# Kernel tuning notes

Hardware: AMD Instinct MI355X
Metric: run time of the kernel (lower is better)

Reference implementation:

```python
import jax, jax.numpy as jnp
import numpy as np

D = 512
H = 8
DH = D // H  # 64


def setup_inputs() -> dict:
    key = jax.random.key(0)
    ks = jax.random.split(key, 7)
    batch, la, lb = 8, 256, 256
    A = jax.random.normal(ks[0], (batch, la, D), dtype=jnp.float32)
    B = jax.random.normal(ks[1], (batch, lb, D), dtype=jnp.float32)
    s = 1.0 / np.sqrt(D)
    W1 = jax.random.uniform(ks[2], (D, D), minval=-s, maxval=s, dtype=jnp.float32)
    b1 = jax.random.uniform(ks[3], (D,), minval=-s, maxval=s, dtype=jnp.float32)
    W2 = jax.random.uniform(ks[4], (D, D), minval=-s, maxval=s, dtype=jnp.float32)
    b2 = jax.random.uniform(ks[5], (D,), minval=-s, maxval=s, dtype=jnp.float32)
    q = jax.random.normal(ks[6], (DH,), dtype=jnp.float32) * 0.1
    return {"A": A, "B": B, "W1": W1, "b1": b1, "W2": W2, "b2": b2, "q": q}


def reference(A, B, W1, b1, W2, b2, q):
    bs, la, _ = A.shape
    lb = B.shape[1]
    # Linear + ReLU, then raw row-major reshape to (batch, heads, len, dh)
    # (matches torch .view semantics: NOT a head-transpose split)
    A_ = jax.nn.relu(A @ W1.T + b1).reshape(bs, H, la, DH)
    B_ = jax.nn.relu(B @ W2.T + b2).reshape(bs, H, lb, DH)
    # bilinear score: tanh of elementwise pairwise product, dotted with q
    # att_maps: [bs, H, la, lb]
    att_maps = jnp.einsum(
        "bhijc,c->bhij",
        jnp.tanh(A_[:, :, :, None, :] * B_[:, :, None, :, :]),
        q,
    )
    temp_b2a = jax.nn.softmax(jnp.mean(att_maps, axis=3), axis=2)  # [bs,H,la]
    temp_a2b = jax.nn.softmax(jnp.mean(att_maps, axis=2), axis=2)  # [bs,H,lb]
    A_heads = A.reshape(bs, H, la, DH)
    B_heads = B.reshape(bs, H, lb, DH)
    A_p = jnp.sum(A_heads * temp_b2a[..., None], axis=2).reshape(bs, -1)  # [bs, d]
    B_p = jnp.sum(B_heads * temp_a2b[..., None], axis=2).reshape(bs, -1)  # [bs, d]
    return (
        jnp.concatenate((A_p, B_p), axis=1),
        jnp.mean(temp_b2a, axis=1),
        jnp.mean(temp_a2b, axis=1),
    )
```

## Files before the change

kernel.cpp:

```cpp
#include <hip/hip_runtime.h>
#include <hip/hip_bf16.h>

#define LOG2E 1.4426950408889634f
#define CHEB_R 4.0f
#define CHEB_M 40
#define CHEB_P 80
#define PI_F 3.14159265358979f

typedef __attribute__((ext_vector_type(8))) short short8b;
typedef __attribute__((ext_vector_type(4))) short short4b;
typedef __attribute__((ext_vector_type(4))) float f32x4;

__device__ __forceinline__ float fast_exp2(float x) {
#if __has_builtin(__builtin_amdgcn_exp2f)
  return __builtin_amdgcn_exp2f(x);
#else
  return exp2f(x);
#endif
}
__device__ __forceinline__ float fast_rcp(float x) {
#if __has_builtin(__builtin_amdgcn_rcpf)
  return __builtin_amdgcn_rcpf(x);
#else
  return 1.0f / x;
#endif
}
__device__ __forceinline__ short f2bf(float f) {
  __hip_bfloat16 h = __float2bfloat16(f);
  return *reinterpret_cast<short*>(&h);
}

__global__ __launch_bounds__(256) void gemm_kernel(
    const float* __restrict__ Xa, const float* __restrict__ Wa,
    const float* __restrict__ ba, float* __restrict__ Oa,
    const float* __restrict__ Xb, const float* __restrict__ Wb,
    const float* __restrict__ bb, float* __restrict__ Ob) {
  const int isB = blockIdx.z;
  const float* X = isB ? Xb : Xa;
  const float* W = isB ? Wb : Wa;
  const float* bias = isB ? bb : ba;
  float* O = isB ? Ob : Oa;

  __shared__ __align__(16) short As[64 * 40];
  __shared__ __align__(16) short Ws[64 * 40];

  int t = threadIdx.x;
  int m0 = blockIdx.x * 64, n0 = blockIdx.y * 64;
  int l = t & 63, w = t >> 6;
  int wm = (w >> 1) * 32, wn = (w & 1) * 32;
  int lr = l & 15, ko = (l >> 4) * 8;

  f32x4 acc[2][2];
#pragma unroll
  for (int m = 0; m < 2; ++m)
#pragma unroll
    for (int n = 0; n < 2; ++n) acc[m][n] = f32x4{0.f, 0.f, 0.f, 0.f};

  for (int k0 = 0; k0 < 512; k0 += 32) {
#pragma unroll
    for (int s = 0; s < 2; ++s) {
      int slot = t + s * 256;
      int row = slot >> 3, qd = (slot & 7) << 2;
      float4 v = *reinterpret_cast<const float4*>(&X[(m0 + row) * 512 + k0 + qd]);
      short4b sv = {f2bf(v.x), f2bf(v.y), f2bf(v.z), f2bf(v.w)};
      *reinterpret_cast<short4b*>(&As[row * 40 + qd]) = sv;
      float4 u = *reinterpret_cast<const float4*>(&W[(n0 + row) * 512 + k0 + qd]);
      short4b su = {f2bf(u.x), f2bf(u.y), f2bf(u.z), f2bf(u.w)};
      *reinterpret_cast<short4b*>(&Ws[row * 40 + qd]) = su;
    }
    __syncthreads();

    short8b afr[2], bfr[2];
#pragma unroll
    for (int m = 0; m < 2; ++m)
      afr[m] = *reinterpret_cast<const short8b*>(&As[(wm + m * 16 + lr) * 40 + ko]);
#pragma unroll
    for (int n = 0; n < 2; ++n)
      bfr[n] = *reinterpret_cast<const short8b*>(&Ws[(wn + n * 16 + lr) * 40 + ko]);
#pragma unroll
    for (int m = 0; m < 2; ++m)
#pragma unroll
      for (int n = 0; n < 2; ++n)
        acc[m][n] = __builtin_amdgcn_mfma_f32_16x16x32_bf16(afr[m], bfr[n], acc[m][n], 0, 0, 0);
    __syncthreads();
  }

#pragma unroll
  for (int n = 0; n < 2; ++n) {
    int col = n0 + wn + n * 16 + lr;
    float bv = bias[col];
#pragma unroll
    for (int m = 0; m < 2; ++m) {
      int rbase = m0 + wm + m * 16 + (l >> 4) * 4;
#pragma unroll
      for (int r = 0; r < 4; ++r) {
        float v = acc[m][n][r] + bv;
        O[(rbase + r) * 512 + col] = v > 0.f ? v : 0.f;
      }
    }
  }
}

__global__ __launch_bounds__(256) void moments_kernel(
    const float* __restrict__ Ar, const float* __restrict__ Br,
    float* __restrict__ Fpart, float* __restrict__ Gpart,
    float* __restrict__ cmn) {
  __shared__ __align__(16) float smem[13056];

  int t = threadIdx.x;

  if (blockIdx.x == 64) {
    if (blockIdx.y != 0 || blockIdx.z != 0) return;
    float* S = smem;
    float* T = smem + 6400;
    float* H = smem + 9600;
    for (int e = t; e < 6400; e += 256) {
      int p = e >> 6 ? e / 80 : e / 80;
      p = e / 80;
      int qq = e - p * 80;
      float xp = CHEB_R * 0.5f * (1.f + cosf((2.f * p + 1.f) * (PI_F / 160.f)));
      float xq = CHEB_R * 0.5f * (1.f + cosf((2.f * qq + 1.f) * (PI_F / 160.f)));
      S[e] = tanhf(xp * xq);
    }
    for (int e = t; e < CHEB_M * 80; e += 256) {
      int n = e / 80, qq = e - n * 80;
      T[e] = cosf((float)n * (2.f * qq + 1.f) * (PI_F / 160.f));
    }
    __syncthreads();
    for (int e = t; e < CHEB_M * 80; e += 256) {
      int n = e / 80, p = e - n * 80;
      float s = 0.f;
      for (int qq = 0; qq < 80; ++qq) s = fmaf(T[n * 80 + qq], S[p * 80 + qq], s);
      H[n * 80 + p] = s;
    }
    __syncthreads();
    for (int e = t; e < CHEB_M * CHEB_M; e += 256) {
      int m = e / CHEB_M, n = e - m * CHEB_M;
      float s = 0.f;
      for (int p = 0; p < 80; ++p) s = fmaf(T[m * 80 + p], H[n * 80 + p], s);
      float wm = (m == 0) ? 1.f : 2.f;
      float wn = (n == 0) ? 1.f : 2.f;
      cmn[e] = s * (wm * wn / 6400.f);
    }
    return;
  }

  float* red = smem;
  int bh = blockIdx.x, half = blockIdx.y, quad = blockIdx.z;
  const float* X = half ? Br : Ar;
  float* Out = half ? Gpart : Fpart;
  int c = t & 63, colsel = t >> 6;
  int colhi = quad * 2 + (colsel & 1);
  int rowh = colsel >> 1;
  int rbase = (bh >> 3) * 256 + (bh & 7) * 32 + rowh * 16;
  const float* p = X + rbase * 512 + colhi * 64 + c;

  float acc[CHEB_M];
#pragma unroll
  for (int m = 0; m < CHEB_M; ++m) acc[m] = 0.f;

#pragma unroll 1
  for (int rr = 0; rr < 16; ++rr) {
    float a = p[rr * 512];
    float u = fminf(a * (2.f / CHEB_R) - 1.f, 1.f);
    float tp = 1.f, tc = u;
    acc[0] += 1.f;
    acc[1] += u;
#pragma unroll
    for (int m = 2; m < CHEB_M; ++m) {
      float tn = fmaf(2.f * u, tc, -tp);
      acc[m] += tn;
      tp = tc; tc = tn;
    }
  }
#pragma unroll
  for (int m = 0; m < CHEB_M; ++m) red[(colsel * CHEB_M + m) * 64 + c] = acc[m];
  __syncthreads();
  for (int e = t; e < CHEB_M * 64; e += 256) {
    int m = e >> 6, cc = e & 63;
    float s = red[(0 * CHEB_M + m) * 64 + cc] + red[(1 * CHEB_M + m) * 64 + cc] +
              red[(2 * CHEB_M + m) * 64 + cc] + red[(3 * CHEB_M + m) * 64 + cc];
    Out[(((bh * 4 + quad) * CHEB_M) + m) * 64 + cc] = s;
  }
}

__global__ __launch_bounds__(512) void finalize_kernel(
    const float* __restrict__ Ar, const float* __restrict__ Br,
    const float* __restrict__ Fpart, const float* __restrict__ Gpart,
    const float* __restrict__ cmn, const float* __restrict__ q,
    float* __restrict__ rowmean, float* __restrict__ colmean) {
  __shared__ float cs[CHEB_M * CHEB_M];
  __shared__ float Fs[CHEB_M * 64];
  __shared__ float Gs[CHEB_M * 64];
  __shared__ float gq[CHEB_M * 64];
  __shared__ float dq[CHEB_M * 64];

  int bh = blockIdx.x, qd = blockIdx.y;
  int t = threadIdx.x;

  for (int e = t; e < CHEB_M * CHEB_M; e += 512) cs[e] = cmn[e];
  for (int e = t; e < CHEB_M * 64; e += 512) {
    float f = 0.f, g = 0.f;
#pragma unroll
    for (int p = 0; p < 4; ++p) {
      f += Fpart[((bh * 4 + p) * CHEB_M) * 64 + e];
      g += Gpart[((bh * 4 + p) * CHEB_M) * 64 + e];
    }
    Fs[e] = f; Gs[e] = g;
  }
  __syncthreads();

  for (int e = t; e < CHEB_M * 64; e += 512) {
    int m = e >> 6, c = e & 63;
    float qc = q[c] * (1.f / 256.f);
    float sg = 0.f, sd = 0.f;
    for (int n = 0; n < CHEB_M; ++n) {
      sg = fmaf(cs[m * CHEB_M + n], Gs[n * 64 + c], sg);
      sd = fmaf(cs[n * CHEB_M + m], Fs[n * 64 + c], sd);
    }
    gq[e] = sg * qc;
    dq[e] = sd * qc;
  }
  __syncthreads();

  int rbase = (bh >> 3) * 256 + (bh & 7) * 32;
  {
    int i = qd * 64 + (t >> 3);
    int ce = t & 7;
    const float* base = Ar + (rbase + (i >> 3)) * 512 + (i & 7) * 64;
    float s = 0.f;
#pragma unroll 1
    for (int cc = 0; cc < 8; ++cc) {
      int c = ce * 8 + cc;
      float a = base[c];
      float u = fminf(a * (2.f / CHEB_R) - 1.f, 1.f);
      float tp = 1.f, tc = u;
      s += gq[0 * 64 + c];
      s = fmaf(gq[1 * 64 + c], u, s);
#pragma unroll
      for (int m = 2; m < CHEB_M; ++m) {
        float tn = fmaf(2.f * u, tc, -tp);
        s = fmaf(gq[m * 64 + c], tn, s);
        tp = tc; tc = tn;
      }
    }
    s += __shfl_xor(s, 1);
    s += __shfl_xor(s, 2);
    s += __shfl_xor(s, 4);
    if ((t & 7) == 0) rowmean[bh * 256 + i] = s;
  }
  {
    int j = qd * 64 + (t >> 3);
    int ce = t & 7;
    const float* base = Br + (rbase + (j >> 3)) * 512 + (j & 7) * 64;
    float s = 0.f;
#pragma unroll 1
    for (int cc = 0; cc < 8; ++cc) {
      int c = ce * 8 + cc;
      float b = base[c];
      float u = fminf(b * (2.f / CHEB_R) - 1.f, 1.f);
      float tp = 1.f, tc = u;
      s += dq[0 * 64 + c];
      s = fmaf(dq[1 * 64 + c], u, s);
#pragma unroll
      for (int m = 2; m < CHEB_M; ++m) {
        float tn = fmaf(2.f * u, tc, -tp);
        s = fmaf(dq[m * 64 + c], tn, s);
        tp = tc; tc = tn;
      }
    }
    s += __shfl_xor(s, 1);
    s += __shfl_xor(s, 2);
    s += __shfl_xor(s, 4);
    if ((t & 7) == 0) colmean[bh * 256 + j] = s;
  }
}

__global__ __launch_bounds__(512) void softmax_pool_kernel(
    const float* __restrict__ rowmean, const float* __restrict__ colmean,
    const float* __restrict__ A0, const float* __restrict__ B0,
    float* __restrict__ b2a, float* __restrict__ a2b,
    float* __restrict__ poolA, float* __restrict__ poolB) {
  int bh = blockIdx.x, chunk = blockIdx.y;
  int b = bh >> 3, h = bh & 7;
  int t = threadIdx.x;
  int tt = t & 255;
  int lane = t & 63, w = (t >> 6) & 3;
  __shared__ float redA[4], redB[4], redC[4], redD[4];
  __shared__ float tA[256], tB[256];
  __shared__ float pp[8][64];

  float r = rowmean[bh * 256 + tt];
  float cs = colmean[bh * 256 + tt];

  float mr = r, mc = cs;
#pragma unroll
  for (int off = 32; off >= 1; off >>= 1) {
    mr = fmaxf(mr, __shfl_xor(mr, off));
    mc = fmaxf(mc, __shfl_xor(mc, off));
  }
  if (lane == 0) { redA[w] = mr; redB[w] = mc; }
  __syncthreads();
  mr = fmaxf(fmaxf(redA[0], redA[1]), fmaxf(redA[2], redA[3]));
  mc = fmaxf(fmaxf(redB[0], redB[1]), fmaxf(redB[2], redB[3]));

  float er = fast_exp2((r - mr) * LOG2E);
  float ec = fast_exp2((cs - mc) * LOG2E);
  float sr = er, sc = ec;
#pragma unroll
  for (int off = 32; off >= 1; off >>= 1) {
    sr += __shfl_xor(sr, off);
    sc += __shfl_xor(sc, off);
  }
  if (lane == 0) { redC[w] = sr; redD[w] = sc; }
  __syncthreads();
  sr = redC[0] + redC[1] + redC[2] + redC[3];
  sc = redD[0] + redD[1] + redD[2] + redD[3];

  float vb2a = er * fast_rcp(sr);
  float va2b = ec * fast_rcp(sc);
  tA[tt] = vb2a; tB[tt] = va2b;
  if (chunk == 0) {
    b2a[bh * 256 + tt] = vb2a;
    a2b[bh * 256 + tt] = va2b;
  }
  __syncthreads();

  int c = t & 63, isub = t >> 6;
  const float* Ab = A0 + b * 131072 + h * 16384;
  const float* Bb = B0 + b * 131072 + h * 16384;
  float pa = 0.f, pb = 0.f;
#pragma unroll
  for (int ii = 0; ii < 8; ++ii) {
    int i = chunk * 64 + isub * 8 + ii;
    pa = fmaf(Ab[i * 64 + c], tA[i], pa);
    pb = fmaf(Bb[i * 64 + c], tB[i], pb);
  }
  pp[isub][c] = pa;
  __syncthreads();
  if (t < 64) {
    float s = 0.f;
#pragma unroll
    for (int k = 0; k < 8; ++k) s += pp[k][t];
    poolA[(bh * 4 + chunk) * 64 + t] = s;
  }
  __syncthreads();
  pp[isub][c] = pb;
  __syncthreads();
  if (t < 64) {
    float s = 0.f;
#pragma unroll
    for (int k = 0; k < 8; ++k) s += pp[k][t];
    poolB[(bh * 4 + chunk) * 64 + t] = s;
  }
}

__global__ __launch_bounds__(256) void final_kernel(
    const float* __restrict__ poolA, const float* __restrict__ poolB,
    const float* __restrict__ b2a, const float* __restrict__ a2b,
    float* __restrict__ out) {
  int b = blockIdx.x, t = threadIdx.x;
  float s1 = 0.f, s2 = 0.f;
#pragma unroll
  for (int h = 0; h < 8; ++h) {
    s1 += b2a[(b * 8 + h) * 256 + t];
    s2 += a2b[(b * 8 + h) * 256 + t];
  }
  out[8192 + b * 256 + t] = s1 * 0.125f;
  out[10240 + b * 256 + t] = s2 * 0.125f;

#pragma unroll
  for (int hh = 0; hh < 2; ++hh) {
    int idx = hh * 256 + t;
    int h = idx >> 6, c = idx & 63;
    int base = ((b * 8 + h) * 4) * 64 + c;
    float sA = poolA[base] + poolA[base + 64] + poolA[base + 128] + poolA[base + 192];
    float sB = poolB[base] + poolB[base + 64] + poolB[base + 128] + poolB[base + 192];
    out[b * 1024 + h * 64 + c] = sA;
    out[b * 1024 + 512 + h * 64 + c] = sB;
  }
}

extern "C" void kernel_launch(void* const* d_in, const int* in_sizes, int n_in,
                              void* d_out, int out_size, void* d_ws, size_t ws_size,
                              hipStream_t stream) {
  const float* A  = (const float*)d_in[0];
  const float* B  = (const float*)d_in[1];
  const float* W1 = (const float*)d_in[2];
  const float* b1 = (const float*)d_in[3];
  const float* W2 = (const float*)d_in[4];
  const float* b2 = (const float*)d_in[5];
  const float* q  = (const float*)d_in[6];
  float* out = (float*)d_out;
  float* ws = (float*)d_ws;

  float* Ar      = ws;
  float* Br      = ws + 1048576;
  float* Fpart   = ws + 2097152;
  float* Gpart   = ws + 2752512;
  float* cmn     = ws + 3407872;
  float* rowmean = ws + 3409472;
  float* colmean = ws + 3425856;
  float* b2a     = ws + 3442240;
  float* a2b     = ws + 3458624;
  float* poolA   = ws + 3475008;
  float* poolB   = ws + 3491392;

  gemm_kernel<<<dim3(32, 8, 2), 256, 0, stream>>>(A, W1, b1, Ar, B, W2, b2, Br);
  moments_kernel<<<dim3(65, 2, 4), 256, 0, stream>>>(Ar, Br, Fpart, Gpart, cmn);
  finalize_kernel<<<dim3(64, 4), 512, 0, stream>>>(Ar, Br, Fpart, Gpart, cmn, q,
                                                   rowmean, colmean);
  softmax_pool_kernel<<<dim3(64, 4), 512, 0, stream>>>(
      rowmean, colmean, A, B, b2a, a2b, poolA, poolB);
  final_kernel<<<8, 256, 0, stream>>>(poolA, poolB, b2a, a2b, out);
}
```

Before: 70.99 us.

## Move Chebyshev coefficient setup into GEMM launch and interleave recurrences for ILP

The one-block computation of the tanh Chebyshev coefficient matrix moves from the moments kernel into an extra z-slice of the GEMM launch. It now runs alongside the GEMM and no longer trails behind moments blocks, and tanhf is replaced by an exp2/rcp form. The moments and finalize kernels now evaluate four independent Chebyshev recurrences at once instead of one serial chain, which raises instruction-level parallelism. The GEMM kernel's shared memory grows to about 51KB to hold the coefficient scratch, which may lower GEMM occupancy.

```diff
diff --git a/kernel.cpp b/kernel.cpp
--- a/kernel.cpp
+++ b/kernel.cpp
@@ -2,9 +2,9 @@
 #include <hip/hip_bf16.h>
 
 #define LOG2E 1.4426950408889634f
+#define SC2   2.8853900817779268f
 #define CHEB_R 4.0f
 #define CHEB_M 40
-#define CHEB_P 80
 #define PI_F 3.14159265358979f
 
 typedef __attribute__((ext_vector_type(8))) short short8b;
@@ -30,21 +30,61 @@
   return *reinterpret_cast<short*>(&h);
 }
 
-__global__ __launch_bounds__(256) void gemm_kernel(
+__global__ __launch_bounds__(256) void gemm_coef_kernel(
     const float* __restrict__ Xa, const float* __restrict__ Wa,
     const float* __restrict__ ba, float* __restrict__ Oa,
     const float* __restrict__ Xb, const float* __restrict__ Wb,
-    const float* __restrict__ bb, float* __restrict__ Ob) {
+    const float* __restrict__ bb, float* __restrict__ Ob,
+    float* __restrict__ cmn) {
+  __shared__ __align__(16) char smem_raw[51712];
+  int t = threadIdx.x;
+
+  if (blockIdx.z == 2) {
+    if (blockIdx.x != 0 || blockIdx.y != 0) return;
+    float* S = (float*)smem_raw;
+    float* T = S + 6400;
+    float* H = S + 9600;
+    float* xn = S + 12800;
+    if (t < 80) xn[t] = CHEB_R * 0.5f * (1.f + cosf((2.f * t + 1.f) * (PI_F / 160.f)));
+    __syncthreads();
+    for (int e = t; e < 6400; e += 256) {
+      int p = e / 80, qq = e - p * 80;
+      float x = xn[p] * xn[qq];
+      float ee = fast_exp2(x * SC2);
+      S[e] = (ee - 1.f) * fast_rcp(ee + 1.f);
+    }
+    for (int e = t; e < CHEB_M * 80; e += 256) {
+      int n = e / 80, qq = e - n * 80;
+      T[e] = cosf((float)n * (2.f * qq + 1.f) * (PI_F / 160.f));
+    }
+    __syncthreads();
+    for (int e = t; e < CHEB_M * 80; e += 256) {
+      int n = e / 80, p = e - n * 80;
+      float s = 0.f;
+      for (int qq = 0; qq < 80; ++qq) s = fmaf(T[n * 80 + qq], S[p * 80 + qq], s);
+      H[n * 80 + p] = s;
+    }
+    __syncthreads();
+    for (int e = t; e < CHEB_M * CHEB_M; e += 256) {
+      int m = e / CHEB_M, n = e - m * CHEB_M;
+      float s = 0.f;
+      for (int p = 0; p < 80; ++p) s = fmaf(T[m * 80 + p], H[n * 80 + p], s);
+      float wm = (m == 0) ? 1.f : 2.f;
+      float wn = (n == 0) ? 1.f : 2.f;
+      cmn[e] = s * (wm * wn / 6400.f);
+    }
+    return;
+  }
+
   const int isB = blockIdx.z;
   const float* X = isB ? Xb : Xa;
   const float* W = isB ? Wb : Wa;
   const float* bias = isB ? bb : ba;
   float* O = isB ? Ob : Oa;
 
-  __shared__ __align__(16) short As[64 * 40];
-  __shared__ __align__(16) short Ws[64 * 40];
-
-  int t = threadIdx.x;
+  short* As = (short*)smem_raw;
+  short* Ws = As + 64 * 40;
+
   int m0 = blockIdx.x * 64, n0 = blockIdx.y * 64;
   int l = t & 63, w = t >> 6;
   int wm = (w >> 1) * 32, wn = (w & 1) * 32;
@@ -103,49 +143,9 @@
 
 __global__ __launch_bounds__(256) void moments_kernel(
     const float* __restrict__ Ar, const float* __restrict__ Br,
-    float* __restrict__ Fpart, float* __restrict__ Gpart,
-    float* __restrict__ cmn) {
-  __shared__ __align__(16) float smem[13056];
-
+    float* __restrict__ Fpart, float* __restrict__ Gpart) {
+  __shared__ float red[4 * CHEB_M * 64];
   int t = threadIdx.x;
-
-  if (blockIdx.x == 64) {
-    if (blockIdx.y != 0 || blockIdx.z != 0) return;
-    float* S = smem;
-    float* T = smem + 6400;
-    float* H = smem + 9600;
-    for (int e = t; e < 6400; e += 256) {
-      int p = e >> 6 ? e / 80 : e / 80;
-      p = e / 80;
-      int qq = e - p * 80;
-      float xp = CHEB_R * 0.5f * (1.f + cosf((2.f * p + 1.f) * (PI_F / 160.f)));
-      float xq = CHEB_R * 0.5f * (1.f + cosf((2.f * qq + 1.f) * (PI_F / 160.f)));
-      S[e] = tanhf(xp * xq);
-    }
-    for (int e = t; e < CHEB_M * 80; e += 256) {
-      int n = e / 80, qq = e - n * 80;
-      T[e] = cosf((float)n * (2.f * qq + 1.f) * (PI_F / 160.f));
-    }
-    __syncthreads();
-    for (int e = t; e < CHEB_M * 80; e += 256) {
-      int n = e / 80, p = e - n * 80;
-      float s = 0.f;
-      for (int qq = 0; qq < 80; ++qq) s = fmaf(T[n * 80 + qq], S[p * 80 + qq], s);
-      H[n * 80 + p] = s;
-    }
-    __syncthreads();
-    for (int e = t; e < CHEB_M * CHEB_M; e += 256) {
-      int m = e / CHEB_M, n = e - m * CHEB_M;
-      float s = 0.f;
-      for (int p = 0; p < 80; ++p) s = fmaf(T[m * 80 + p], H[n * 80 + p], s);
-      float wm = (m == 0) ? 1.f : 2.f;
-      float wn = (n == 0) ? 1.f : 2.f;
-      cmn[e] = s * (wm * wn / 6400.f);
-    }
-    return;
-  }
-
-  float* red = smem;
   int bh = blockIdx.x, half = blockIdx.y, quad = blockIdx.z;
   const float* X = half ? Br : Ar;
   float* Out = half ? Gpart : Fpart;
@@ -160,17 +160,28 @@
   for (int m = 0; m < CHEB_M; ++m) acc[m] = 0.f;
 
 #pragma unroll 1
-  for (int rr = 0; rr < 16; ++rr) {
-    float a = p[rr * 512];
-    float u = fminf(a * (2.f / CHEB_R) - 1.f, 1.f);
-    float tp = 1.f, tc = u;
-    acc[0] += 1.f;
-    acc[1] += u;
+  for (int rr = 0; rr < 16; rr += 4) {
+    float a0 = p[(rr + 0) * 512];
+    float a1 = p[(rr + 1) * 512];
+    float a2 = p[(rr + 2) * 512];
+    float a3 = p[(rr + 3) * 512];
+    float u0 = fminf(a0 * 0.5f - 1.f, 1.f);
+    float u1 = fminf(a1 * 0.5f - 1.f, 1.f);
+    float u2 = fminf(a2 * 0.5f - 1.f, 1.f);
+    float u3 = fminf(a3 * 0.5f - 1.f, 1.f);
+    acc[0] += 4.f;
+    acc[1] += (u0 + u1) + (u2 + u3);
+    float tp0 = 1.f, tc0 = u0, tp1 = 1.f, tc1 = u1;
+    float tp2 = 1.f, tc2 = u2, tp3 = 1.f, tc3 = u3;
 #pragma unroll
     for (int m = 2; m < CHEB_M; ++m) {
-      float tn = fmaf(2.f * u, tc, -tp);
-      acc[m] += tn;
-      tp = tc; tc = tn;
+      float tn0 = fmaf(2.f * u0, tc0, -tp0);
+      float tn1 = fmaf(2.f * u1, tc1, -tp1);
+      float tn2 = fmaf(2.f * u2, tc2, -tp2);
+      float tn3 = fmaf(2.f * u3, tc3, -tp3);
+      acc[m] += (tn0 + tn1) + (tn2 + tn3);
+      tp0 = tc0; tc0 = tn0; tp1 = tc1; tc1 = tn1;
+      tp2 = tc2; tc2 = tn2; tp3 = tc3; tc3 = tn3;
     }
   }
 #pragma unroll
@@ -227,23 +238,39 @@
   {
     int i = qd * 64 + (t >> 3);
     int ce = t & 7;
-    const float* base = Ar + (rbase + (i >> 3)) * 512 + (i & 7) * 64;
-    float s = 0.f;
-#pragma unroll 1
-    for (int cc = 0; cc < 8; ++cc) {
-      int c = ce * 8 + cc;
-      float a = base[c];
-      float u = fminf(a * (2.f / CHEB_R) - 1.f, 1.f);
-      float tp = 1.f, tc = u;
-      s += gq[0 * 64 + c];
-      s = fmaf(gq[1 * 64 + c], u, s);
+    const float* base = Ar + (rbase + (i >> 3)) * 512 + (i & 7) * 64 + ce * 8;
+    float s0 = 0.f, s1 = 0.f, s2 = 0.f, s3 = 0.f;
+#pragma unroll
+    for (int g4 = 0; g4 < 2; ++g4) {
+      int c0 = ce * 8 + g4 * 4;
+      float a0 = base[g4 * 4 + 0], a1 = base[g4 * 4 + 1];
+      float a2 = base[g4 * 4 + 2], a3 = base[g4 * 4 + 3];
+      float u0 = fminf(a0 * 0.5f - 1.f, 1.f);
+      float u1 = fminf(a1 * 0.5f - 1.f, 1.f);
+      float u2 = fminf(a2 * 0.5f - 1.f, 1.f);
+      float u3 = fminf(a3 * 0.5f - 1.f, 1.f);
+      s0 += gq[c0 + 0]; s1 += gq[c0 + 1]; s2 += gq[c0 + 2]; s3 += gq[c0 + 3];
+      s0 = fmaf(gq[64 + c0 + 0], u0, s0);
+      s1 = fmaf(gq[64 + c0 + 1], u1, s1);
+      s2 = fmaf(gq[64 + c0 + 2], u2, s2);
+      s3 = fmaf(gq[64 + c0 + 3], u3, s3);
+      float tp0 = 1.f, tc0 = u0, tp1 = 1.f, tc1 = u1;
+      float tp2 = 1.f, tc2 = u2, tp3 = 1.f, tc3 = u3;
 #pragma unroll
       for (int m = 2; m < CHEB_M; ++m) {
-        float tn = fmaf(2.f * u, tc, -tp);
-        s = fmaf(gq[m * 64 + c], tn, s);
-        tp = tc; tc = tn;
+        float tn0 = fmaf(2.f * u0, tc0, -tp0);
+        float tn1 = fmaf(2.f * u1, tc1, -tp1);
+        float tn2 = fmaf(2.f * u2, tc2, -tp2);
+        float tn3 = fmaf(2.f * u3, tc3, -tp3);
+        s0 = fmaf(gq[m * 64 + c0 + 0], tn0, s0);
+        s1 = fmaf(gq[m * 64 + c0 + 1], tn1, s1);
+        s2 = fmaf(gq[m * 64 + c0 + 2], tn2, s2);
+        s3 = fmaf(gq[m * 64 + c0 + 3], tn3, s3);
+        tp0 = tc0; tc0 = tn0; tp1 = tc1; tc1 = tn1;
+        tp2 = tc2; tc2 = tn2; tp3 = tc3; tc3 = tn3;
       }
     }
+    float s = (s0 + s1) + (s2 + s3);
     s += __shfl_xor(s, 1);
     s += __shfl_xor(s, 2);
     s += __shfl_xor(s, 4);
@@ -252,23 +279,39 @@
   {
     int j = qd * 64 + (t >> 3);
     int ce = t & 7;
-    const float* base = Br + (rbase + (j >> 3)) * 512 + (j & 7) * 64;
-    float s = 0.f;
-#pragma unroll 1
-    for (int cc = 0; cc < 8; ++cc) {
-      int c = ce * 8 + cc;
-      float b = base[c];
-      float u = fminf(b * (2.f / CHEB_R) - 1.f, 1.f);
-      float tp = 1.f, tc = u;
-      s += dq[0 * 64 + c];
-      s = fmaf(dq[1 * 64 + c], u, s);
+    const float* base = Br + (rbase + (j >> 3)) * 512 + (j & 7) * 64 + ce * 8;
+    float s0 = 0.f, s1 = 0.f, s2 = 0.f, s3 = 0.f;
+#pragma unroll
+    for (int g4 = 0; g4 < 2; ++g4) {
+      int c0 = ce * 8 + g4 * 4;
+      float a0 = base[g4 * 4 + 0], a1 = base[g4 * 4 + 1];
+      float a2 = base[g4 * 4 + 2], a3 = base[g4 * 4 + 3];
+      float u0 = fminf(a0 * 0.5f - 1.f, 1.f);
+      float u1 = fminf(a1 * 0.5f - 1.f, 1.f);
+      float u2 = fminf(a2 * 0.5f - 1.f, 1.f);
+      float u3 = fminf(a3 * 0.5f - 1.f, 1.f);
+      s0 += dq[c0 + 0]; s1 += dq[c0 + 1]; s2 += dq[c0 + 2]; s3 += dq[c0 + 3];
+      s0 = fmaf(dq[64 + c0 + 0], u0, s0);
+      s1 = fmaf(dq[64 + c0 + 1], u1, s1);
+      s2 = fmaf(dq[64 + c0 + 2], u2, s2);
+      s3 = fmaf(dq[64 + c0 + 3], u3, s3);
+      float tp0 = 1.f, tc0 = u0, tp1 = 1.f, tc1 = u1;
+      float tp2 = 1.f, tc2 = u2, tp3 = 1.f, tc3 = u3;
 #pragma unroll
       for (int m = 2; m < CHEB_M; ++m) {
-        float tn = fmaf(2.f * u, tc, -tp);
-        s = fmaf(dq[m * 64 + c], tn, s);
-        tp = tc; tc = tn;
+        float tn0 = fmaf(2.f * u0, tc0, -tp0);
+        float tn1 = fmaf(2.f * u1, tc1, -tp1);
+        float tn2 = fmaf(2.f * u2, tc2, -tp2);
+        float tn3 = fmaf(2.f * u3, tc3, -tp3);
+        s0 = fmaf(dq[m * 64 + c0 + 0], tn0, s0);
+        s1 = fmaf(dq[m * 64 + c0 + 1], tn1, s1);
+        s2 = fmaf(dq[m * 64 + c0 + 2], tn2, s2);
+        s3 = fmaf(dq[m * 64 + c0 + 3], tn3, s3);
+        tp0 = tc0; tc0 = tn0; tp1 = tc1; tc1 = tn1;
+        tp2 = tc2; tc2 = tn2; tp3 = tc3; tc3 = tn3;
       }
     }
+    float s = (s0 + s1) + (s2 + s3);
     s += __shfl_xor(s, 1);
     s += __shfl_xor(s, 2);
     s += __shfl_xor(s, 4);
@@ -406,8 +449,9 @@
   float* poolA   = ws + 3475008;
   float* poolB   = ws + 3491392;
 
-  gemm_kernel<<<dim3(32, 8, 2), 256, 0, stream>>>(A, W1, b1, Ar, B, W2, b2, Br);
-  moments_kernel<<<dim3(65, 2, 4), 256, 0, stream>>>(Ar, Br, Fpart, Gpart, cmn);
+  gemm_coef_kernel<<<dim3(32, 8, 3), 256, 0, stream>>>(
+      A, W1, b1, Ar, B, W2, b2, Br, cmn);
+  moments_kernel<<<dim3(64, 2, 4), 256, 0, stream>>>(Ar, Br, Fpart, Gpart);
   finalize_kernel<<<dim3(64, 4), 512, 0, stream>>>(Ar, Br, Fpart, Gpart, cmn, q,
                                                    rowmean, colmean);
   softmax_pool_kernel<<<dim3(64, 4), 512, 0, stream>>>(
```

New measurement: 69.54 us. 1.02x faster.
